# Performance work log

Hardware: AMD Instinct MI355X
Metric: run time of the kernel (lower is better)

Reference implementation:

```python
import jax, jax.numpy as jnp
import numpy as np

N = 16777216
C = 2
BINS = 10
MOMENTUM = 0.75


def setup_inputs() -> dict:
    key = jax.random.key(0)
    k1, k2 = jax.random.split(key)
    outputs = jax.random.normal(k1, (N, C), dtype=jnp.float32)
    targets = jax.random.randint(k2, (N,), 0, C, dtype=jnp.int64)
    acc_sum = jnp.zeros((BINS,), dtype=jnp.float32)
    return {"outputs": outputs, "targets": targets, "acc_sum": acc_sum}


def reference(outputs, targets, acc_sum):
    n, c = outputs.shape
    tgt = targets.astype(jnp.int32)
    logp = jax.nn.log_softmax(outputs, axis=1)            # [N, C]
    p_t = jnp.take_along_axis(jnp.exp(logp), tgt[:, None], axis=1)[:, 0]
    # |softmax - onehot| summed over classes == 2 * (1 - p_target)
    g = 2.0 * (1.0 - p_t)                                 # [N], in [0, 2]
    # torch loop covers edges linspace(0,1,bins+1): only g in [0, 1) gets a weight
    bin_idx = jnp.clip(jnp.floor(g * BINS).astype(jnp.int32), 0, BINS - 1)
    valid = g < 1.0
    counts = jax.ops.segment_sum(jnp.where(valid, 1.0, 0.0).astype(jnp.float32),
                                 bin_idx, num_segments=BINS)  # [BINS]
    # acc_sum updated only for non-empty bins (EMA with momentum)
    new_acc = jnp.where(counts > 0, MOMENTUM * acc_sum + (1.0 - MOMENTUM) * counts, acc_sum)
    per_sample_acc = new_acc[bin_idx]
    weights = jnp.where(valid & (counts[bin_idx] > 0),
                        jnp.float32(n) / per_sample_acc,
                        jnp.float32(0.0))                 # [N]
    # cross_entropy(reduction='none') = -log_softmax[target]
    loss = -jnp.take_along_axis(logp, tgt[:, None], axis=1)[:, 0]
    return jnp.mean(loss * weights)
```

## Files before the change

kernel.cpp:

```cpp
#include <hip/hip_runtime.h>

#define BINS   10
#define CSHIFT 26
#define QMASK  0x03FFFFFFu
#define QSCALE 2097152.0f
#define QLN2   1453635.25f
#define GRID   1536
#define TPB    256
#define TILE   1024


__global__ void ghm_zero_ws(unsigned* ws) {
    if (threadIdx.x < 320) ws[threadIdx.x] = 0u;
}

__device__ __forceinline__ void gld_lds16(const void* g, void* l) {
    __builtin_amdgcn_global_load_lds(
        (const __attribute__((address_space(1))) void*)g,
        (__attribute__((address_space(3))) void*)l, 16, 0, 0);
}

__device__ __forceinline__ void proc1(float o0, float o1, int t, unsigned* A) {
    const float Th[BINS] = {
        2.9444390f, 2.1972246f, 1.7346011f, 1.3862944f, 1.0986123f,
        0.8472979f, 0.6190392f, 0.4054651f, 0.2006707f, 0.0f };
    float s = o0 - o1;
    float d = __int_as_float(__float_as_int(s) ^ (t << 31));
    float em = __expf(-d);
    float qf = fmaf(__log2f(1.0f + em), QLN2, 0.5f);
    unsigned val = (unsigned)qf + (1u << CSHIFT);
    #pragma unroll
    for (int b = 0; b < BINS; ++b)
        A[b] += (d > Th[b]) ? val : 0u;
}

__global__ __launch_bounds__(TPB, 6)
void ghm_main(const float* __restrict__ outs,
              const int*   __restrict__ tgt,
              unsigned char* __restrict__ ws,
              int n, int use_slots) {
    __shared__ union {
        struct {
            unsigned char o[2][TILE * 8];
            unsigned char t[2][TILE * 4];
        } st;
        struct {
            unsigned h[BINS][256];
            unsigned c[BINS][16];
            float    q[BINS][16];
        } ep;
    } sh;

    const int tid  = threadIdx.x;
    const int lane = tid & 63;
    const int wv   = tid >> 6;

    unsigned A[BINS];
    #pragma unroll
    for (int b = 0; b < BINS; ++b) A[b] = 0u;

    const int ntiles = n >> 10;

    const char* outs_b = (const char*)outs;
    const char* tgt_b  = (const char*)tgt;
    #define STAGE(tile, pb)                                                     \
        do {                                                                    \
            const char* go = outs_b + ((size_t)(tile) << 13) + (wv << 11)       \
                             + (lane << 4);                                     \
            char*       lo = (char*)sh.st.o[pb] + (wv << 11);                   \
            gld_lds16(go, lo);                                                  \
            gld_lds16(go + 1024, lo + 1024);                                    \
            const char* gt = tgt_b + ((size_t)(tile) << 12) + (wv << 10)        \
                             + (lane << 4);                                     \
            gld_lds16(gt, (char*)sh.st.t[pb] + (wv << 10));                     \
        } while (0)

    int t  = blockIdx.x;
    int pb = 0;
    if (t < ntiles) STAGE(t, 0);
    __syncthreads();

    for (; t < ntiles; t += gridDim.x) {
        int tn = t + gridDim.x;
        if (tn < ntiles) STAGE(tn, pb ^ 1);

        const float4* o4 = (const float4*)sh.st.o[pb];
        const int4*   t4 = (const int4*)sh.st.t[pb];
        float4 a  = o4[2 * tid];
        float4 bq = o4[2 * tid + 1];
        int4   tv = t4[tid];
        proc1(a.x,  a.y,  tv.x, A);
        proc1(a.z,  a.w,  tv.y, A);
        proc1(bq.x, bq.y, tv.z, A);
        proc1(bq.z, bq.w, tv.w, A);

        __syncthreads();
        pb ^= 1;
    }

    int rem = ntiles << 10;
    if (blockIdx.x == 0) {
        for (int s = rem + tid; s < n; s += TPB)
            proc1(outs[2 * s], outs[2 * s + 1], tgt[s], A);
    }

    __syncthreads();
    #pragma unroll
    for (int b = 0; b < BINS; ++b) sh.ep.h[b][tid] = A[b];
    __syncthreads();

    if (tid < 16 * BINS) {
        int bin  = tid >> 4;
        int part = tid & 15;
        unsigned c = 0, q = 0;
        #pragma unroll
        for (int j = 0; j < 16; ++j) {
            unsigned v = sh.ep.h[bin][j * 16 + part];
            c += v >> CSHIFT;
            q += v & QMASK;
        }
        sh.ep.c[bin][part] = c;
        sh.ep.q[bin][part] = (float)q;
    }
    __syncthreads();
    if (tid < BINS) {
        unsigned c = 0; float q = 0.0f;
        #pragma unroll
        for (int j = 0; j < 16; ++j) { c += sh.ep.c[tid][j]; q += sh.ep.q[tid][j]; }
        if (use_slots) {
            ((unsigned*)ws)[tid * GRID + blockIdx.x]        = c;
            ((float*)ws)[(BINS + tid) * GRID + blockIdx.x]  = q * (1.0f / QSCALE);
        } else if (c) {
            atomicAdd((unsigned*)(ws + 128 * tid + 64), c);
            atomicAdd((float*)   (ws + 128 * tid),      q * (1.0f / QSCALE));
        }
    }
}

__global__ __launch_bounds__(256)
void ghm_final2(const unsigned char* __restrict__ ws,
                const float* __restrict__ acc_sum,
                float* __restrict__ out) {
    __shared__ unsigned lc[BINS][256];
    __shared__ float    lq[BINS][256];
    __shared__ unsigned sc[BINS][16];
    __shared__ float    sq[BINS][16];
    const int tid = threadIdx.x;
    const unsigned* cb = (const unsigned*)ws;
    const float*    qb = (const float*)ws + (size_t)BINS * GRID;

    unsigned c[BINS]; float q[BINS];
    #pragma unroll
    for (int b = 0; b < BINS; ++b) { c[b] = 0u; q[b] = 0.0f; }
    for (int r = tid; r < GRID; r += 256) {
        #pragma unroll
        for (int b = 0; b < BINS; ++b) {
            c[b] += cb[b * GRID + r];
            q[b] += qb[b * GRID + r];
        }
    }
    #pragma unroll
    for (int b = 0; b < BINS; ++b) { lc[b][tid] = c[b]; lq[b][tid] = q[b]; }
    __syncthreads();

    if (tid < 16 * BINS) {
        int bin = tid >> 4, part = tid & 15;
        unsigned cc = 0u; float cq = 0.0f;
        #pragma unroll
        for (int j = 0; j < 16; ++j) {
            cc += lc[bin][j * 16 + part];
            cq += lq[bin][j * 16 + part];
        }
        sc[bin][part] = cc;
        sq[bin][part] = cq;
    }
    __syncthreads();

    if (tid == 0) {
        float r = 0.0f, pq = 0.0f;
        unsigned pc = 0u;
        #pragma unroll
        for (int b = 0; b < BINS; ++b) {
            unsigned cc = 0u; float cq = 0.0f;
            #pragma unroll
            for (int j = 0; j < 16; ++j) { cc += sc[b][j]; cq += sq[b][j]; }
            unsigned cnt = cc - pc;
            float    qs  = cq - pq;
            pc = cc; pq = cq;
            if (cnt > 0u) {
                float na = 0.75f * acc_sum[b] + 0.25f * (float)cnt;
                r += qs / na;
            }
        }
        *out = r;
    }
}

__global__ void ghm_final(const unsigned char* __restrict__ ws,
                          const float* __restrict__ acc_sum,
                          float* __restrict__ out) {
    if (threadIdx.x == 0) {
        float r = 0.0f, pq = 0.0f;
        unsigned pc = 0u;
        #pragma unroll
        for (int b = 0; b < BINS; ++b) {
            float    cq = *(const float*)   (ws + 128 * b);
            unsigned cc = *(const unsigned*)(ws + 128 * b + 64);
            unsigned cnt = cc - pc;
            float    qs  = cq - pq;
            pc = cc; pq = cq;
            if (cnt > 0u) {
                float na = 0.75f * acc_sum[b] + 0.25f * (float)cnt;
                r += qs / na;
            }
        }
        *out = r;
    }
}

extern "C" void kernel_launch(void* const* d_in, const int* in_sizes, int n_in,
                              void* d_out, int out_size, void* d_ws, size_t ws_size,
                              hipStream_t stream) {
    const float* outputs = (const float*)d_in[0];
    const int*   targets = (const int*)d_in[1];
    const float* acc_sum = (const float*)d_in[2];
    int n = in_sizes[1];

    const int use_slots = (ws_size >= (size_t)2 * BINS * GRID * 4) ? 1 : 0;

    if (!use_slots)
        ghm_zero_ws<<<1, 512, 0, stream>>>((unsigned*)d_ws);
    ghm_main<<<GRID, TPB, 0, stream>>>(outputs, targets,
                                       (unsigned char*)d_ws, n, use_slots);
    if (use_slots)
        ghm_final2<<<1, 256, 0, stream>>>((const unsigned char*)d_ws, acc_sum,
                                          (float*)d_out);
    else
        ghm_final<<<1, 64, 0, stream>>>((const unsigned char*)d_ws, acc_sum,
                                        (float*)d_out);
}
```

Measured before the change: 242.9 us.

## Give each wave its own LDS double-buffer ring and drop block barriers

Restructures the staging loop so each wavefront owns a private double-buffered LDS ring and processes 256-element tiles independently. It synchronises with vmcnt waits instead of block-wide __syncthreads. The aim is to remove barrier stalls between waves and let each wave keep its own prefetch in flight. The trade-offs are smaller per-wave tiles and one redundant prefetch of tile 0 on the last iteration. It also relies on LDS writes from the global-to-LDS loads becoming visible after the vmcnt wait without an explicit barrier.

```diff
diff --git a/kernel.cpp b/kernel.cpp
--- a/kernel.cpp
+++ b/kernel.cpp
@@ -7,7 +7,6 @@
 #define QLN2   1453635.25f
 #define GRID   1536
 #define TPB    256
-#define TILE   1024
 
 
 __global__ void ghm_zero_ws(unsigned* ws) {
@@ -39,11 +38,8 @@
               const int*   __restrict__ tgt,
               unsigned char* __restrict__ ws,
               int n, int use_slots) {
-    __shared__ union {
-        struct {
-            unsigned char o[2][TILE * 8];
-            unsigned char t[2][TILE * 4];
-        } st;
+    __shared__ __align__(16) union {
+        unsigned char ring[4][2][3072];
         struct {
             unsigned h[BINS][256];
             unsigned c[BINS][16];
@@ -59,46 +55,49 @@
     #pragma unroll
     for (int b = 0; b < BINS; ++b) A[b] = 0u;
 
-    const int ntiles = n >> 10;
+    const int NT = n >> 8;
+    const int NW = gridDim.x << 2;
+    const int gw = (blockIdx.x << 2) + wv;
 
     const char* outs_b = (const char*)outs;
     const char* tgt_b  = (const char*)tgt;
-    #define STAGE(tile, pb)                                                     \
+    unsigned char* r0 = sh.ring[wv][0];
+    unsigned char* r1 = sh.ring[wv][1];
+
+    #define STAGE(tile, rp)                                                     \
         do {                                                                    \
-            const char* go = outs_b + ((size_t)(tile) << 13) + (wv << 11)       \
-                             + (lane << 4);                                     \
-            char*       lo = (char*)sh.st.o[pb] + (wv << 11);                   \
-            gld_lds16(go, lo);                                                  \
-            gld_lds16(go + 1024, lo + 1024);                                    \
-            const char* gt = tgt_b + ((size_t)(tile) << 12) + (wv << 10)        \
-                             + (lane << 4);                                     \
-            gld_lds16(gt, (char*)sh.st.t[pb] + (wv << 10));                     \
+            const char* go = outs_b + ((size_t)(tile) << 11) + (lane << 4);     \
+            gld_lds16(go,        (char*)(rp));                                  \
+            gld_lds16(go + 1024, (char*)(rp) + 1024);                           \
+            gld_lds16(tgt_b + ((size_t)(tile) << 10) + (lane << 4),             \
+                      (char*)(rp) + 2048);                                      \
         } while (0)
 
-    int t  = blockIdx.x;
-    int pb = 0;
-    if (t < ntiles) STAGE(t, 0);
-    __syncthreads();
-
-    for (; t < ntiles; t += gridDim.x) {
-        int tn = t + gridDim.x;
-        if (tn < ntiles) STAGE(tn, pb ^ 1);
-
-        const float4* o4 = (const float4*)sh.st.o[pb];
-        const int4*   t4 = (const int4*)sh.st.t[pb];
-        float4 a  = o4[2 * tid];
-        float4 bq = o4[2 * tid + 1];
-        int4   tv = t4[tid];
-        proc1(a.x,  a.y,  tv.x, A);
-        proc1(a.z,  a.w,  tv.y, A);
-        proc1(bq.x, bq.y, tv.z, A);
-        proc1(bq.z, bq.w, tv.w, A);
-
-        __syncthreads();
-        pb ^= 1;
-    }
-
-    int rem = ntiles << 10;
+    int t = gw;
+    if (t < NT) {
+        STAGE(t, r0);
+        int cur = 0;
+        for (; t < NT; t += NW) {
+            int tn = t + NW;
+            if (tn >= NT) tn = 0;
+            STAGE(tn, cur ? r0 : r1);
+            asm volatile("s_waitcnt vmcnt(3)" ::: "memory");
+            __builtin_amdgcn_sched_barrier(0);
+            const unsigned char* rp = cur ? r1 : r0;
+            const float4* o4 = (const float4*)rp;
+            const int4*   t4 = (const int4*)(rp + 2048);
+            float4 a  = o4[2 * lane];
+            float4 bq = o4[2 * lane + 1];
+            int4   tv = t4[lane];
+            proc1(a.x,  a.y,  tv.x, A);
+            proc1(a.z,  a.w,  tv.y, A);
+            proc1(bq.x, bq.y, tv.z, A);
+            proc1(bq.z, bq.w, tv.w, A);
+            cur ^= 1;
+        }
+    }
+
+    int rem = NT << 8;
     if (blockIdx.x == 0) {
         for (int s = rem + tid; s < n; s += TPB)
             proc1(outs[2 * s], outs[2 * s + 1], tgt[s], A);
```

After: 244.3 us. No clear change (+0.6%).
